# Performance work log

Hardware: AMD Instinct MI355X
Metric: run time of the kernel (lower is better)

## Reference

```python
import jax, jax.numpy as jnp
import numpy as np
import math

B, C, H, W, P = 8, 64, 256, 256, 16


def _conv2d(x, w, groups=1):
    # x: [B,C,H,W], w: [O, I/groups, kh, kw], 'SAME' padding, stride 1
    return jax.lax.conv_general_dilated(
        x, w, window_strides=(1, 1), padding='SAME',
        dimension_numbers=('NCHW', 'OIHW', 'NCHW'),
        feature_group_count=groups)


def _bn(x, g, b, m, v, eps=1e-5):
    # inference-mode BatchNorm2d over channel dim
    inv = jax.lax.rsqrt(v + eps)
    return (x - m[None, :, None, None]) * (g * inv)[None, :, None, None] + b[None, :, None, None]


def _layernorm(x, g, b, eps=1e-5):
    mu = x.mean(-1, keepdims=True)
    var = ((x - mu) ** 2).mean(-1, keepdims=True)
    return (x - mu) * jax.lax.rsqrt(var + eps) * g + b


def setup_inputs() -> dict:
    key = jax.random.key(0)
    ks = jax.random.split(key, 16)
    feat_map = jax.random.normal(ks[0], (B, C, H, W), jnp.float32)
    query = jax.random.normal(ks[1], (B, P, C), jnp.float32)
    key_tokens = jax.random.normal(ks[2], (B, H * W, C), jnp.float32)
    s = 1.0 / math.sqrt(C)
    dw_w = jax.random.normal(ks[3], (C, 1, 3, 3), jnp.float32) * (1.0 / 3.0)
    pw_w = jax.random.normal(ks[4], (C, C, 1, 1), jnp.float32) * s
    bn1_g = jnp.ones((C,)); bn1_b = jnp.zeros((C,))
    bn1_m = jnp.zeros((C,)); bn1_v = jnp.ones((C,))
    bn2_g = jnp.ones((C,)); bn2_b = jnp.zeros((C,))
    bn2_m = jnp.zeros((C,)); bn2_v = jnp.ones((C,))
    aff_w = jax.random.normal(ks[5], (P, C), jnp.float32) * s
    loc_w1 = jax.random.normal(ks[6], (C, C), jnp.float32) * s
    loc_b1 = jnp.zeros((C,))
    loc_w2 = jax.random.normal(ks[7], (C, C), jnp.float32) * s
    loc_b2 = jnp.zeros((C,))
    glb_w1 = jax.random.normal(ks[8], (C, C), jnp.float32) * s
    glb_b1 = jnp.zeros((C,))
    glb_w2 = jax.random.normal(ks[9], (C, C), jnp.float32) * s
    glb_b2 = jnp.zeros((C,))
    ln_g = jnp.ones((C,)); ln_b = jnp.zeros((C,))
    topo_scale = jnp.float32(0.01)
    orient_scale = jnp.float32(0.01)
    angles = jnp.linspace(0.0, math.pi, P + 1)[:-1]
    proto_orient = jnp.stack([jnp.cos(2.0 * angles), jnp.sin(2.0 * angles)], axis=1).astype(jnp.float32)
    return dict(feat_map=feat_map, query=query, key_tokens=key_tokens,
                dw_w=dw_w, bn1_g=bn1_g, bn1_b=bn1_b, bn1_m=bn1_m, bn1_v=bn1_v,
                pw_w=pw_w, bn2_g=bn2_g, bn2_b=bn2_b, bn2_m=bn2_m, bn2_v=bn2_v,
                aff_w=aff_w,
                loc_w1=loc_w1, loc_b1=loc_b1, loc_w2=loc_w2, loc_b2=loc_b2,
                glb_w1=glb_w1, glb_b1=glb_b1, glb_w2=glb_w2, glb_b2=glb_b2,
                ln_g=ln_g, ln_b=ln_b, topo_scale=topo_scale, orient_scale=orient_scale,
                proto_orient=proto_orient)


def reference(feat_map, query, key_tokens,
              dw_w, bn1_g, bn1_b, bn1_m, bn1_v,
              pw_w, bn2_g, bn2_b, bn2_m, bn2_v,
              aff_w,
              loc_w1, loc_b1, loc_w2, loc_b2,
              glb_w1, glb_b1, glb_w2, glb_b2,
              ln_g, ln_b, topo_scale, orient_scale, proto_orient):
    b, c, h, w = feat_map.shape
    hw = h * w
    # conv_spatial: depthwise 3x3 -> BN -> ReLU -> 1x1 -> BN -> ReLU
    x = _conv2d(feat_map, dw_w, groups=c)
    x = jax.nn.relu(_bn(x, bn1_g, bn1_b, bn1_m, bn1_v))
    x = _conv2d(x, pw_w)
    x = jax.nn.relu(_bn(x, bn2_g, bn2_b, bn2_m, bn2_v))
    feat_conv = x.reshape(b, c, hw).transpose(0, 2, 1)  # [B, L, C]
    # Sobel edge magnitude on channel-mean map
    edge_input = feat_map.mean(axis=1, keepdims=True)  # [B,1,H,W]
    sob_x = jnp.array([[-1, 0, 1], [-2, 0, 2], [-1, 0, 1]], jnp.float32).reshape(1, 1, 3, 3)
    sob_y = jnp.array([[-1, -2, -1], [0, 0, 0], [1, 2, 1]], jnp.float32).reshape(1, 1, 3, 3)
    gx = _conv2d(edge_input, sob_x)
    gy = _conv2d(edge_input, sob_y)
    edge_strength = jnp.sqrt(gx * gx + gy * gy + 1e-6)  # [B,1,H,W]
    # standardized edge weight over tokens (unbiased std, matching torch.std)
    ew = edge_strength.reshape(b, hw, 1)
    ew_mean = ew.mean(axis=1, keepdims=True)
    ew_var = ((ew - ew_mean) ** 2).sum(axis=1, keepdims=True) / (hw - 1)
    edge_weight = (ew - ew_mean) / (jnp.sqrt(ew_var) + 1e-5)  # [B,L,1]
    # doubled-angle orientation encoding
    gx2 = gx * gx
    gy2 = gy * gy
    denom = gx2 + gy2 + 1e-6
    ori_x = (gx2 - gy2) / denom
    ori_y = 2.0 * gx * gy / denom
    orient_tokens = jnp.concatenate([ori_x, ori_y], axis=1).reshape(b, 2, hw).transpose(0, 2, 1)  # [B,L,2]
    edge_conf = edge_strength.reshape(b, hw, 1)
    edge_conf = edge_conf / (edge_conf.mean(axis=1, keepdims=True) + 1e-6)
    edge_conf = jnp.clip(edge_conf, 0.0, 3.0)
    # prototype orientation bias
    proto_dirs = proto_orient / jnp.maximum(
        jnp.linalg.norm(proto_orient, axis=-1, keepdims=True), 1e-12)
    orient_scores = jnp.einsum('blc,pc->blp', orient_tokens, proto_dirs)
    orient_bias = orient_scores * edge_conf  # [B,L,P]
    raw_affinity = jnp.einsum('blc,pc->blp', feat_conv, aff_w)
    affinity_logits = raw_affinity + topo_scale * edge_weight + orient_scale * orient_bias
    affinity = jax.nn.softmax(affinity_logits, axis=1)  # softmax over tokens L
    prototypes = jnp.einsum('blp,blc->bpc', affinity, key_tokens)  # [B,P,C]
    # Contextual Significance Weighting gate
    z = prototypes + query
    loc = jax.nn.relu(z @ loc_w1.T + loc_b1) @ loc_w2.T + loc_b2
    g_ctx = z.mean(axis=1, keepdims=True)
    glb = jax.nn.relu(g_ctx @ glb_w1.T + glb_b1) @ glb_w2.T + glb_b2
    attn_weights = jax.nn.sigmoid(loc + glb)
    out = _layernorm(query * attn_weights + query, ln_g, ln_b)
    return out
```

## Files before the change

kernel.cpp:

```cpp
#include <hip/hip_runtime.h>
#include <hip/hip_fp16.h>
#include <math.h>

#define HW     65536
#define WIDTH  256
#define HEIGHT 256

typedef __attribute__((ext_vector_type(8))) short bf16x8;
typedef __attribute__((ext_vector_type(4))) float f32x4;

__device__ __forceinline__ float relu_f(float x){ return x > 0.f ? x : 0.f; }
__device__ __forceinline__ unsigned int f2bf(float x){
    union { float f; unsigned int u; } v; v.f = x;
    unsigned int r = v.u + 0x7fffu + ((v.u >> 16) & 1u);
    return r >> 16;
}
__device__ __forceinline__ float bfbits2f(unsigned int lo16){
    union { unsigned int u; float f; } v; v.u = lo16 << 16; return v.f;
}
__device__ __forceinline__ float h2f(unsigned int bits16){
    __half h = *(__half*)&bits16; return __half2float(h);
}

__global__ void k_prep(const float* __restrict__ pw_w, const float* __restrict__ aff_w,
                       const float* __restrict__ g1, const float* __restrict__ b1,
                       const float* __restrict__ m1, const float* __restrict__ v1,
                       const float* __restrict__ g2, const float* __restrict__ b2,
                       const float* __restrict__ m2, const float* __restrict__ v2,
                       float* __restrict__ scsh, unsigned short* __restrict__ pwA,
                       unsigned short* __restrict__ affA){
    int t = threadIdx.x;
    for (int i = t; i < 4096; i += 256){
        int e = i & 7, l = (i >> 3) & 63, ks = (i >> 9) & 1, ct = i >> 10;
        int co = ct * 16 + (l & 15);
        int ci = ks * 32 + (l >> 4) * 8 + e;
        pwA[i] = (unsigned short)f2bf(pw_w[co * 64 + ci]);
    }
    for (int i = t; i < 1024; i += 256){
        int e = i & 7, l = (i >> 3) & 63, ks = i >> 9;
        int p = l & 15, k = ks * 32 + (l >> 4) * 8 + e;
        affA[i] = (unsigned short)f2bf(aff_w[p * 64 + k]);
    }
    if (t < 64){
        float s = g1[t] * rsqrtf(v1[t] + 1e-5f);
        scsh[t]       = s;
        scsh[64 + t]  = b1[t] - m1[t] * s;
        float s2 = g2[t] * rsqrtf(v2[t] + 1e-5f);
        scsh[128 + t] = s2;
        scsh[192 + t] = b2[t] - m2[t] * s2;
    }
}

__global__ __launch_bounds__(256, 4) void k_conv_aff(
    const float* __restrict__ feat, const float* __restrict__ dw_w,
    const float* __restrict__ scsh, const unsigned short* __restrict__ pwA,
    const unsigned short* __restrict__ affA,
    unsigned short* __restrict__ logitsH, float* __restrict__ ei)
{
    __shared__ unsigned short x1u[256 * 68];
    __shared__ float eibuf[4][256];
    int t = threadIdx.x;
    int lane = t & 63;
    int wu = __builtin_amdgcn_readfirstlane(t >> 6);
    int orig = blockIdx.x;
    int flat = (orig & 7) * 256 + (orig >> 3);
    int b = flat >> 8, h = flat & 255;

    const bf16x8* pwA8 = (const bf16x8*)pwA;
    bf16x8 apw0 = pwA8[(wu * 2 + 0) * 64 + lane];
    bf16x8 apw1 = pwA8[(wu * 2 + 1) * 64 + lane];
    const bf16x8* affA8 = (const bf16x8*)affA;
    bf16x8 aaf0 = affA8[lane];
    bf16x8 aaf1 = affA8[64 + lane];
    int lcol = lane & 15, pq = lane >> 4;
    int cb = wu * 16 + pq * 4;
    float4 sc2v = *(const float4*)(scsh + 128 + cb);
    float4 sh2v = *(const float4*)(scsh + 192 + cb);

    int px0 = lane * 4;
    const float* fb = feat + (size_t)b * 64 * HW;
    int hh0 = (h > 0) ? h - 1 : 0;
    int hh2 = (h < 255) ? h + 1 : 255;
    float rw0 = (h > 0) ? 1.f : 0.f;
    float rw2 = (h < 255) ? 1.f : 0.f;
    int   roff0 = hh0 * WIDTH, roff1 = h * WIDTH, roff2 = hh2 * WIDTH;
    float mx = 0.f, my = 0.f, mz = 0.f, mw = 0.f;
    int swz = ((lane >> 2) & 7) << 1;
    #pragma unroll
    for (int cp = 0; cp < 8; cp++){
        int ci0 = wu * 16 + cp * 2;
        int ci1 = ci0 + 1;
        const float* base0 = fb + (size_t)ci0 * HW + px0;
        const float* base1 = fb + (size_t)ci1 * HW + px0;
        float a00=0.f,a01=0.f,a02=0.f,a03=0.f, a10=0.f,a11=0.f,a12=0.f,a13=0.f;
        #pragma unroll
        for (int r = 0; r < 3; r++){
            int roff = (r == 0) ? roff0 : ((r == 1) ? roff1 : roff2);
            float rwf = (r == 0) ? rw0 : ((r == 1) ? 1.f : rw2);
            float4 v0 = *(const float4*)(base0 + roff);
            float4 v1 = *(const float4*)(base1 + roff);
            float w00 = dw_w[ci0*9 + r*3 + 0] * rwf;
            float w01 = dw_w[ci0*9 + r*3 + 1] * rwf;
            float w02 = dw_w[ci0*9 + r*3 + 2] * rwf;
            float w10 = dw_w[ci1*9 + r*3 + 0] * rwf;
            float w11 = dw_w[ci1*9 + r*3 + 1] * rwf;
            float w12 = dw_w[ci1*9 + r*3 + 2] * rwf;
            float lf0 = __shfl_up(v0.w, 1);  if (lane == 0)  lf0 = 0.f;
            float rt0 = __shfl_down(v0.x, 1); if (lane == 63) rt0 = 0.f;
            float lf1 = __shfl_up(v1.w, 1);  if (lane == 0)  lf1 = 0.f;
            float rt1 = __shfl_down(v1.x, 1); if (lane == 63) rt1 = 0.f;
            a00 += lf0*w00 + v0.x*w01 + v0.y*w02;
            a01 += v0.x*w00 + v0.y*w01 + v0.z*w02;
            a02 += v0.y*w00 + v0.z*w01 + v0.w*w02;
            a03 += v0.z*w00 + v0.w*w01 + rt0*w02;
            a10 += lf1*w10 + v1.x*w11 + v1.y*w12;
            a11 += v1.x*w10 + v1.y*w11 + v1.z*w12;
            a12 += v1.y*w10 + v1.z*w11 + v1.w*w12;
            a13 += v1.z*w10 + v1.w*w11 + rt1*w12;
            if (r == 1){
                mx += v0.x + v1.x; my += v0.y + v1.y;
                mz += v0.z + v1.z; mw += v0.w + v1.w;
            }
        }
        float s0 = scsh[ci0], o0 = scsh[64 + ci0];
        float s1 = scsh[ci1], o1 = scsh[64 + ci1];
        int dwi = ((wu * 8 + cp) ^ swz) * 2;
        unsigned int pk0 = f2bf(relu_f(fmaf(a00,s0,o0))) | (f2bf(relu_f(fmaf(a10,s1,o1))) << 16);
        unsigned int pk1 = f2bf(relu_f(fmaf(a01,s0,o0))) | (f2bf(relu_f(fmaf(a11,s1,o1))) << 16);
        unsigned int pk2 = f2bf(relu_f(fmaf(a02,s0,o0))) | (f2bf(relu_f(fmaf(a12,s1,o1))) << 16);
        unsigned int pk3 = f2bf(relu_f(fmaf(a03,s0,o0))) | (f2bf(relu_f(fmaf(a13,s1,o1))) << 16);
        *(unsigned int*)&x1u[(px0 + 0) * 68 + dwi] = pk0;
        *(unsigned int*)&x1u[(px0 + 1) * 68 + dwi] = pk1;
        *(unsigned int*)&x1u[(px0 + 2) * 68 + dwi] = pk2;
        *(unsigned int*)&x1u[(px0 + 3) * 68 + dwi] = pk3;
    }
    *(float4*)&eibuf[wu][px0] = make_float4(mx, my, mz, mw);
    __syncthreads();
    {
        float m = (eibuf[0][t] + eibuf[1][t]) + (eibuf[2][t] + eibuf[3][t]);
        ei[(size_t)b * HW + h * WIDTH + t] = m * (1.f / 64.f);
    }

    int k0d = pq * 4;
    #pragma unroll
    for (int half = 0; half < 2; half++){
        f32x4 accB[8];
        #pragma unroll
        for (int q = 0; q < 8; q++){
            int jt = half * 8 + q;
            int swzj = (jt & 7) << 1;
            const unsigned short* rowp = &x1u[(jt * 16 + lcol) * 68];
            union { bf16x8 v; uint2 u[2]; } b0, b1;
            b0.u[0] = *(const uint2*)&rowp[((k0d)          ^ swzj) * 2];
            b0.u[1] = *(const uint2*)&rowp[((k0d + 2)      ^ swzj) * 2];
            b1.u[0] = *(const uint2*)&rowp[((16 + k0d)     ^ swzj) * 2];
            b1.u[1] = *(const uint2*)&rowp[((16 + k0d + 2) ^ swzj) * 2];
            f32x4 acc = {0.f, 0.f, 0.f, 0.f};
            acc = __builtin_amdgcn_mfma_f32_16x16x32_bf16(apw0, b0.v, acc, 0, 0, 0);
            acc = __builtin_amdgcn_mfma_f32_16x16x32_bf16(apw1, b1.v, acc, 0, 0, 0);
            accB[q] = acc;
        }
        __syncthreads();
        #pragma unroll
        for (int q = 0; q < 8; q++){
            int jt = half * 8 + q;
            int swzj = (jt & 7) << 1;
            f32x4 acc = accB[q];
            unsigned int y0 = f2bf(relu_f(fmaf(acc[0], sc2v.x, sh2v.x)))
                            | (f2bf(relu_f(fmaf(acc[1], sc2v.y, sh2v.y))) << 16);
            unsigned int y1 = f2bf(relu_f(fmaf(acc[2], sc2v.z, sh2v.z)))
                            | (f2bf(relu_f(fmaf(acc[3], sc2v.w, sh2v.w))) << 16);
            int D = (wu * 8 + pq * 2) ^ swzj;
            *(uint2*)&x1u[(jt * 16 + lcol) * 68 + D * 2] = make_uint2(y0, y1);
        }
    }
    __syncthreads();

    int p0 = pq * 4;
    #pragma unroll
    for (int q = 0; q < 4; q++){
        int jt = wu * 4 + q;
        int swzj = (jt & 7) << 1;
        const unsigned short* rowp = &x1u[(jt * 16 + lcol) * 68];
        union { bf16x8 v; uint2 u[2]; } b0, b1;
        b0.u[0] = *(const uint2*)&rowp[((k0d)          ^ swzj) * 2];
        b0.u[1] = *(const uint2*)&rowp[((k0d + 2)      ^ swzj) * 2];
        b1.u[0] = *(const uint2*)&rowp[((16 + k0d)     ^ swzj) * 2];
        b1.u[1] = *(const uint2*)&rowp[((16 + k0d + 2) ^ swzj) * 2];
        f32x4 acc = {0.f, 0.f, 0.f, 0.f};
        acc = __builtin_amdgcn_mfma_f32_16x16x32_bf16(aaf0, b0.v, acc, 0, 0, 0);
        acc = __builtin_amdgcn_mfma_f32_16x16x32_bf16(aaf1, b1.v, acc, 0, 0, 0);
        int gx = h * WIDTH + jt * 16 + lcol;
        __half h0 = __float2half(acc[0]), h1v = __float2half(acc[1]);
        __half h2 = __float2half(acc[2]), h3v = __float2half(acc[3]);
        unsigned int u0 = (unsigned int)(*(unsigned short*)&h0)
                        | ((unsigned int)(*(unsigned short*)&h1v) << 16);
        unsigned int u1 = (unsigned int)(*(unsigned short*)&h2)
                        | ((unsigned int)(*(unsigned short*)&h3v) << 16);
        *(uint2*)&logitsH[((size_t)b * HW + gx) * 16 + p0] = make_uint2(u0, u1);
    }
}

__global__ __launch_bounds__(256) void k_sobel_stats(const float* __restrict__ ei,
                                                     float* __restrict__ part){
    int ch = blockIdx.x, b = blockIdx.y, t = threadIdx.x;
    int lane = t & 63, w = t >> 6;
    int h = ch * 4 + w;
    int px0 = lane * 4;
    const float* e = ei + (size_t)b * HW;
    int hh0 = (h > 0) ? h - 1 : 0;
    int hh2 = (h < 255) ? h + 1 : 255;
    float rw0 = (h > 0) ? 1.f : 0.f;
    float rw2 = (h < 255) ? 1.f : 0.f;
    float4 v0 = *(const float4*)(e + hh0 * WIDTH + px0);
    float4 v1 = *(const float4*)(e + h   * WIDTH + px0);
    float4 v2 = *(const float4*)(e + hh2 * WIDTH + px0);
    v0.x *= rw0; v0.y *= rw0; v0.z *= rw0; v0.w *= rw0;
    v2.x *= rw2; v2.y *= rw2; v2.z *= rw2; v2.w *= rw2;
    float l0 = __shfl_up(v0.w, 1);   if (lane == 0)  l0 = 0.f;
    float r0 = __shfl_down(v0.x, 1); if (lane == 63) r0 = 0.f;
    float l1 = __shfl_up(v1.w, 1);   if (lane == 0)  l1 = 0.f;
    float r1 = __shfl_down(v1.x, 1); if (lane == 63) r1 = 0.f;
    float l2 = __shfl_up(v2.w, 1);   if (lane == 0)  l2 = 0.f;
    float r2 = __shfl_down(v2.x, 1); if (lane == 63) r2 = 0.f;
    float t0[6]  = {l0, v0.x, v0.y, v0.z, v0.w, r0};
    float m1a[6] = {l1, v1.x, v1.y, v1.z, v1.w, r1};
    float b2a[6] = {l2, v2.x, v2.y, v2.z, v2.w, r2};
    float s1 = 0.f, s2 = 0.f;
    #pragma unroll
    for (int j = 0; j < 4; j++){
        float gx = (t0[j+2] - t0[j]) + 2.f*(m1a[j+2] - m1a[j]) + (b2a[j+2] - b2a[j]);
        float gy = (b2a[j] + 2.f*b2a[j+1] + b2a[j+2]) - (t0[j] + 2.f*t0[j+1] + t0[j+2]);
        float esv = sqrtf(gx*gx + gy*gy + 1e-6f);
        s1 += esv; s2 += esv * esv;
    }
    #pragma unroll
    for (int off = 32; off >= 1; off >>= 1){
        s1 += __shfl_xor(s1, off, 64);
        s2 += __shfl_xor(s2, off, 64);
    }
    __shared__ float rs1[4], rs2[4];
    if (lane == 0){ rs1[w] = s1; rs2[w] = s2; }
    __syncthreads();
    if (t == 0)
        part[(b*64+ch)*2]     = (rs1[0] + rs1[1]) + (rs1[2] + rs1[3]);
    if (t == 1)
        part[(b*64+ch)*2 + 1] = (rs2[0] + rs2[1]) + (rs2[2] + rs2[3]);
}

__global__ __launch_bounds__(256) void k_smproto(
    const unsigned short* __restrict__ logitsH, const float* __restrict__ ei,
    const float* __restrict__ part, const float* __restrict__ proto_orient,
    const float* __restrict__ topo_s, const float* __restrict__ orient_s,
    const float* __restrict__ key,
    float* __restrict__ smpart, float* __restrict__ ppart)
{
    int ch = blockIdx.x, b = blockIdx.y, t = threadIdx.x;
    __shared__ float eit[4][258];
    __shared__ float sstat[3];
    __shared__ float pdl[32];
    __shared__ float Ml[16];
    __shared__ float rm[4][16], rs[4][16];
    __shared__ unsigned int wlds[512][10];

    for (int i = t; i < 1024; i += 256){
        int r = i >> 8, c = i & 255;
        int row = 2 * ch - 1 + r;
        eit[r][c + 1] = (row >= 0 && row < 256) ? ei[(size_t)b * HW + row * 256 + c] : 0.f;
    }
    if (t >= 128 && t < 136){
        int q = t - 128;
        eit[q >> 1][(q & 1) * 257] = 0.f;
    }
    if (t < 64){
        float s1 = part[(b*64 + t)*2], s2 = part[(b*64 + t)*2 + 1];
        #pragma unroll
        for (int off = 32; off >= 1; off >>= 1){
            s1 += __shfl_xor(s1, off, 64);
            s2 += __shfl_xor(s2, off, 64);
        }
        if (t == 0){
            float mean = s1 / 65536.f;
            float var = (s2 - 65536.f * mean * mean) / 65535.f;
            var = var > 0.f ? var : 0.f;
            sstat[0] = mean;
            sstat[1] = 1.f / (sqrtf(var) + 1e-5f);
            sstat[2] = 1.f / (mean + 1e-6f);
        }
    } else if (t >= 64 && t < 80){
        int p = t - 64;
        float nx = proto_orient[p*2], ny = proto_orient[p*2+1];
        float n = sqrtf(nx*nx + ny*ny);
        n = n > 1e-12f ? n : 1e-12f;
        pdl[p*2] = nx / n; pdl[p*2+1] = ny / n;
    }
    __syncthreads();
    float mean = sstat[0], rstd = sstat[1], cinv = sstat[2];
    float topo = topo_s[0], orient = orient_s[0];

    float m[16], s[16];
    #pragma unroll
    for (int p = 0; p < 16; p++){ m[p] = -1e30f; s[p] = 0.f; }
    uint4 pkA0, pkA1, pkB0, pkB1;
    {
        size_t gl0 = ((size_t)b * HW + ch * 512 + t) * 16;
        size_t gl1 = ((size_t)b * HW + ch * 512 + 256 + t) * 16;
        pkA0 = *(const uint4*)&logitsH[gl0];
        pkA1 = *(const uint4*)&logitsH[gl0 + 8];
        pkB0 = *(const uint4*)&logitsH[gl1];
        pkB1 = *(const uint4*)&logitsH[gl1 + 8];
    }
    float ewv[2], oxv[2], oyv[2];
    #pragma unroll
    for (int i = 0; i < 2; i++){
        int hl = i + 1, w = t;
        float vmm = eit[hl-1][w], vm0 = eit[hl-1][w+1], vmp = eit[hl-1][w+2];
        float v0m = eit[hl][w],                          v0p = eit[hl][w+2];
        float vpm = eit[hl+1][w], vp0 = eit[hl+1][w+1], vpp = eit[hl+1][w+2];
        float gx = vmp - vmm + 2.f*(v0p - v0m) + vpp - vpm;
        float gy = vpm + 2.f*vp0 + vpp - vmm - 2.f*vm0 - vmp;
        float denom = gx*gx + gy*gy + 1e-6f;
        float esv = sqrtf(denom);
        float cf = fminf(fmaxf(esv * cinv, 0.f), 3.f);
        ewv[i] = (esv - mean) * rstd;
        oxv[i] = ((gx*gx - gy*gy) / denom) * cf;
        oyv[i] = (2.f * gx * gy / denom) * cf;
        const uint4& q0 = (i == 0) ? pkA0 : pkB0;
        const uint4& q1 = (i == 0) ? pkA1 : pkB1;
        unsigned int wv[8] = {q0.x, q0.y, q0.z, q0.w, q1.x, q1.y, q1.z, q1.w};
        #pragma unroll
        for (int p = 0; p < 16; p++){
            unsigned int bits = (p & 1) ? (wv[p >> 1] >> 16) : (wv[p >> 1] & 0xffffu);
            float x = h2f(bits) + topo * ewv[i]
                    + orient * (oxv[i]*pdl[p*2] + oyv[i]*pdl[p*2+1]);
            float mn = fmaxf(m[p], x);
            s[p] = s[p] * __expf(m[p] - mn) + __expf(x - mn);
            m[p] = mn;
        }
    }
    #pragma unroll
    for (int p = 0; p < 16; p++){
        #pragma unroll
        for (int off = 32; off >= 1; off >>= 1){
            float m2 = __shfl_xor(m[p], off, 64);
            float s2v = __shfl_xor(s[p], off, 64);
            float mn = fmaxf(m[p], m2);
            s[p] = s[p] * __expf(m[p] - mn) + s2v * __expf(m2 - mn);
            m[p] = mn;
        }
    }
    int wid = t >> 6;
    if ((t & 63) == 0){
        #pragma unroll
        for (int p = 0; p < 16; p++){ rm[wid][p] = m[p]; rs[wid][p] = s[p]; }
    }
    __syncthreads();
    if (t < 16){
        float M = -1e30f, S = 0.f;
        #pragma unroll
        for (int w2 = 0; w2 < 4; w2++){
            float mw = rm[w2][t], sw2 = rs[w2][t];
            float mn = fmaxf(M, mw);
            S = S * __expf(M - mn) + sw2 * __expf(mw - mn);
            M = mn;
        }
        smpart[((b*16 + t)*128 + ch)*2]     = M;
        smpart[((b*16 + t)*128 + ch)*2 + 1] = S;
        Ml[t] = M;
    }
    __syncthreads();
    float Mloc[16];
    #pragma unroll
    for (int p = 0; p < 16; p++) Mloc[p] = Ml[p];

    #pragma unroll
    for (int i = 0; i < 2; i++){
        int tok = i * 256 + t;
        const uint4& q0 = (i == 0) ? pkA0 : pkB0;
        const uint4& q1 = (i == 0) ? pkA1 : pkB1;
        unsigned int wv[8] = {q0.x, q0.y, q0.z, q0.w, q1.x, q1.y, q1.z, q1.w};
        #pragma unroll
        for (int p2 = 0; p2 < 8; p2++){
            int pa = p2*2, pb2 = p2*2 + 1;
            float xa = h2f(wv[p2] & 0xffffu) + topo*ewv[i]
                     + orient*(oxv[i]*pdl[pa*2]  + oyv[i]*pdl[pa*2+1]);
            float xb = h2f(wv[p2] >> 16) + topo*ewv[i]
                     + orient*(oxv[i]*pdl[pb2*2] + oyv[i]*pdl[pb2*2+1]);
            wlds[tok][p2] = f2bf(__expf(xa - Mloc[pa])) | (f2bf(__expf(xb - Mloc[pb2])) << 16);
        }
    }
    __syncthreads();

    int w = t >> 6, lane = t & 63, cg = lane & 15, g = lane >> 4;
    const float4* kp = (const float4*)key + ((size_t)b * HW + ch * 512 + w * 128) * 16;
    float acc[16][4];
    #pragma unroll
    for (int p = 0; p < 16; p++)
        #pragma unroll
        for (int i = 0; i < 4; i++) acc[p][i] = 0.f;
    #pragma unroll 4
    for (int blk = 0; blk < 32; blk++){
        int tok = blk * 4 + g;
        float4 kv = kp[tok * 16 + cg];
        const unsigned int* wp = &wlds[w * 128 + tok][0];
        uint2 q0 = *(const uint2*)&wp[0];
        uint2 q1 = *(const uint2*)&wp[2];
        uint2 q2 = *(const uint2*)&wp[4];
        uint2 q3 = *(const uint2*)&wp[6];
        unsigned int ww[8] = {q0.x, q0.y, q1.x, q1.y, q2.x, q2.y, q3.x, q3.y};
        #pragma unroll
        for (int p2 = 0; p2 < 8; p2++){
            float wa = bfbits2f(ww[p2] & 0xffffu);
            float wb = bfbits2f(ww[p2] >> 16);
            int pa = 2*p2, pb2 = 2*p2 + 1;
            acc[pa][0] = fmaf(wa, kv.x, acc[pa][0]);
            acc[pa][1] = fmaf(wa, kv.y, acc[pa][1]);
            acc[pa][2] = fmaf(wa, kv.z, acc[pa][2]);
            acc[pa][3] = fmaf(wa, kv.w, acc[pa][3]);
            acc[pb2][0] = fmaf(wb, kv.x, acc[pb2][0]);
            acc[pb2][1] = fmaf(wb, kv.y, acc[pb2][1]);
            acc[pb2][2] = fmaf(wb, kv.z, acc[pb2][2]);
            acc[pb2][3] = fmaf(wb, kv.w, acc[pb2][3]);
        }
    }
    #pragma unroll
    for (int p = 0; p < 16; p++)
        #pragma unroll
        for (int i = 0; i < 4; i++){
            acc[p][i] += __shfl_xor(acc[p][i], 16, 64);
            acc[p][i] += __shfl_xor(acc[p][i], 32, 64);
        }
    __syncthreads();
    float (*red)[16][68] = (float (*)[16][68])wlds;
    if (g == 0){
        #pragma unroll
        for (int p = 0; p < 16; p++)
            *(float4*)&red[w][p][cg*4] =
                make_float4(acc[p][0], acc[p][1], acc[p][2], acc[p][3]);
    }
    __syncthreads();
    size_t obase = ((size_t)(b * 128 + ch)) * 1024;
    for (int idx = t; idx < 1024; idx += 256){
        int p = idx >> 6, c = idx & 63;
        ppart[obase + idx] = red[0][p][c] + red[1][p][c] + red[2][p][c] + red[3][p][c];
    }
}

__global__ __launch_bounds__(256) void k_reduce(
    const float* __restrict__ smpart, const float* __restrict__ ppart,
    float* __restrict__ proto)
{
    int p = blockIdx.x, b = blockIdx.y, t = threadIdx.x;
    __shared__ float arr[128], flv[128], partial[4][64];
    float Mt = -1e30f, St = 0.f;
    if (t < 128){
        Mt = smpart[((b*16 + p)*128 + t)*2];
        St = smpart[((b*16 + p)*128 + t)*2 + 1];
        arr[t] = Mt;
    }
    __syncthreads();
    for (int s = 64; s > 0; s >>= 1){
        if (t < s) arr[t] = fmaxf(arr[t], arr[t + s]);
        __syncthreads();
    }
    float M = arr[0];
    __syncthreads();
    if (t < 128) arr[t] = St * __expf(Mt - M);
    __syncthreads();
    for (int s = 64; s > 0; s >>= 1){
        if (t < s) arr[t] += arr[t + s];
        __syncthreads();
    }
    float Stot = arr[0];
    __syncthreads();
    if (t < 128) flv[t] = __expf(Mt - M) / Stot;
    __syncthreads();
    int c = t & 63, half = t >> 6;
    float acc = 0.f;
    #pragma unroll 8
    for (int j = 0; j < 32; j++){
        int ch = half * 32 + j;
        acc += flv[ch] * ppart[((size_t)(b * 128 + ch)) * 1024 + p * 64 + c];
    }
    partial[half][c] = acc;
    __syncthreads();
    if (t < 64)
        proto[b * 1024 + p * 64 + t] =
            (partial[0][t] + partial[1][t]) + (partial[2][t] + partial[3][t]);
}

__global__ __launch_bounds__(256) void k_gate(
    const float* __restrict__ proto, const float* __restrict__ query,
    const float* __restrict__ w1, const float* __restrict__ bb1,
    const float* __restrict__ w2, const float* __restrict__ bb2,
    const float* __restrict__ gw1, const float* __restrict__ gb1,
    const float* __restrict__ gw2, const float* __restrict__ gb2,
    const float* __restrict__ lng, const float* __restrict__ lnb,
    float* __restrict__ out)
{
    __shared__ float z[16][64], h1[16][64], loc[16][64], g[64], hg[64], glb[64];
    int b = blockIdx.x, t = threadIdx.x;
    for (int idx = t; idx < 1024; idx += 256)
        z[idx >> 6][idx & 63] = proto[b * 1024 + idx] + query[b * 1024 + idx];
    __syncthreads();
    for (int idx = t; idx < 1024; idx += 256){
        int p = idx >> 6, j = idx & 63;
        float acc = bb1[j];
        for (int i = 0; i < 64; i++) acc += z[p][i] * w1[j * 64 + i];
        h1[p][j] = relu_f(acc);
    }
    if (t < 64){
        float sg = 0.f;
        for (int p = 0; p < 16; p++) sg += z[p][t];
        g[t] = sg * (1.f / 16.f);
    }
    __syncthreads();
    for (int idx = t; idx < 1024; idx += 256){
        int p = idx >> 6, k = idx & 63;
        float acc = bb2[k];
        for (int j = 0; j < 64; j++) acc += h1[p][j] * w2[k * 64 + j];
        loc[p][k] = acc;
    }
    if (t < 64){
        float acc = gb1[t];
        for (int i = 0; i < 64; i++) acc += g[i] * gw1[t * 64 + i];
        hg[t] = relu_f(acc);
    }
    __syncthreads();
    if (t < 64){
        float acc = gb2[t];
        for (int j = 0; j < 64; j++) acc += hg[j] * gw2[t * 64 + j];
        glb[t] = acc;
    }
    __syncthreads();
    for (int idx = t; idx < 1024; idx += 256){
        int p = idx >> 6, c = idx & 63;
        float a = loc[p][c] + glb[c];
        float sg = 1.f / (1.f + expf(-a));
        float q = query[b * 1024 + idx];
        h1[p][c] = q * sg + q;
    }
    __syncthreads();
    if (t < 16){
        int p = t;
        float mu = 0.f;
        for (int c = 0; c < 64; c++) mu += h1[p][c];
        mu *= (1.f / 64.f);
        float var = 0.f;
        for (int c = 0; c < 64; c++){ float d = h1[p][c] - mu; var += d * d; }
        var *= (1.f / 64.f);
        float rstd = rsqrtf(var + 1e-5f);
        for (int c = 0; c < 64; c++)
            out[b * 1024 + p * 64 + c] = (h1[p][c] - mu) * rstd * lng[c] + lnb[c];
    }
}

extern "C" void kernel_launch(void* const* d_in, const int* in_sizes, int n_in,
                              void* d_out, int out_size, void* d_ws, size_t ws_size,
                              hipStream_t stream){
    (void)in_sizes; (void)n_in; (void)out_size; (void)ws_size;
    const float* feat   = (const float*)d_in[0];
    const float* query  = (const float*)d_in[1];
    const float* key    = (const float*)d_in[2];
    const float* dw_w   = (const float*)d_in[3];
    const float* bn1_g  = (const float*)d_in[4];
    const float* bn1_b  = (const float*)d_in[5];
    const float* bn1_m  = (const float*)d_in[6];
    const float* bn1_v  = (const float*)d_in[7];
    const float* pw_w   = (const float*)d_in[8];
    const float* bn2_g  = (const float*)d_in[9];
    const float* bn2_b  = (const float*)d_in[10];
    const float* bn2_m  = (const float*)d_in[11];
    const float* bn2_v  = (const float*)d_in[12];
    const float* aff_w  = (const float*)d_in[13];
    const float* loc_w1 = (const float*)d_in[14];
    const float* loc_b1 = (const float*)d_in[15];
    const float* loc_w2 = (const float*)d_in[16];
    const float* loc_b2 = (const float*)d_in[17];
    const float* glb_w1 = (const float*)d_in[18];
    const float* glb_b1 = (const float*)d_in[19];
    const float* glb_w2 = (const float*)d_in[20];
    const float* glb_b2 = (const float*)d_in[21];
    const float* ln_g   = (const float*)d_in[22];
    const float* ln_b   = (const float*)d_in[23];
    const float* topo   = (const float*)d_in[24];
    const float* orient = (const float*)d_in[25];
    const float* proto_orient = (const float*)d_in[26];
    float* out = (float*)d_out;
    float* ws  = (float*)d_ws;

    float* ei      = ws;
    unsigned short* logitsH = (unsigned short*)(ws + 1048576);
    float* ppart   = ws + 5242880;
    float* k3part  = ws + 6291456;
    float* smpart  = ws + 6292480;
    float* proto   = ws + 6325248;
    float* scsh    = ws + 6333440;
    unsigned short* pwA  = (unsigned short*)(ws + 6333696);
    unsigned short* affA = (unsigned short*)(ws + 6335744);

    k_prep<<<1, 256, 0, stream>>>(pw_w, aff_w, bn1_g, bn1_b, bn1_m, bn1_v,
                                  bn2_g, bn2_b, bn2_m, bn2_v, scsh, pwA, affA);
    k_conv_aff<<<2048, 256, 0, stream>>>(feat, dw_w, scsh, pwA, affA, logitsH, ei);
    k_sobel_stats<<<dim3(64, 8), 256, 0, stream>>>(ei, k3part);
    k_smproto<<<dim3(128, 8), 256, 0, stream>>>(logitsH, ei, k3part, proto_orient,
                                                topo, orient, key, smpart, ppart);
    k_reduce<<<dim3(16, 8), 256, 0, stream>>>(smpart, ppart, proto);
    k_gate<<<8, 256, 0, stream>>>(proto, query, loc_w1, loc_b1, loc_w2, loc_b2,
                                  glb_w1, glb_b1, glb_w2, glb_b2, ln_g, ln_b, out);
}
```

Measured before the change: 128.2 us.

## Prefetch conv rows, two-pass softmax in smproto, fold reduce into gate kernel

The depthwise conv loop now loads the next channel pair's three rows while the current pair is computed, a register double buffer meant to hide global load latency. k_smproto replaces its online max/sum softmax with a two-pass scheme: a block max first, then exponentials computed once and reused for both the sum and the LDS weights. It also gets a launch-bounds occupancy hint. The separate k_reduce kernel is removed and its cross-chunk softmax merge and prototype reduction move into k_gate, saving a launch but running that reduction over only 8 blocks.

```diff
diff --git a/kernel.cpp b/kernel.cpp
--- a/kernel.cpp
+++ b/kernel.cpp
@@ -86,19 +86,38 @@
     int   roff0 = hh0 * WIDTH, roff1 = h * WIDTH, roff2 = hh2 * WIDTH;
     float mx = 0.f, my = 0.f, mz = 0.f, mw = 0.f;
     int swz = ((lane >> 2) & 7) << 1;
+
+    float4 cur0[3], cur1[3], nxt0[3], nxt1[3];
+    {
+        const float* p0 = fb + (size_t)(wu * 16) * HW + px0;
+        const float* p1 = p0 + HW;
+        cur0[0] = *(const float4*)(p0 + roff0);
+        cur0[1] = *(const float4*)(p0 + roff1);
+        cur0[2] = *(const float4*)(p0 + roff2);
+        cur1[0] = *(const float4*)(p1 + roff0);
+        cur1[1] = *(const float4*)(p1 + roff1);
+        cur1[2] = *(const float4*)(p1 + roff2);
+    }
     #pragma unroll
     for (int cp = 0; cp < 8; cp++){
         int ci0 = wu * 16 + cp * 2;
         int ci1 = ci0 + 1;
-        const float* base0 = fb + (size_t)ci0 * HW + px0;
-        const float* base1 = fb + (size_t)ci1 * HW + px0;
+        if (cp < 7){
+            const float* p0 = fb + (size_t)(ci0 + 2) * HW + px0;
+            const float* p1 = p0 + HW;
+            nxt0[0] = *(const float4*)(p0 + roff0);
+            nxt0[1] = *(const float4*)(p0 + roff1);
+            nxt0[2] = *(const float4*)(p0 + roff2);
+            nxt1[0] = *(const float4*)(p1 + roff0);
+            nxt1[1] = *(const float4*)(p1 + roff1);
+            nxt1[2] = *(const float4*)(p1 + roff2);
+        }
         float a00=0.f,a01=0.f,a02=0.f,a03=0.f, a10=0.f,a11=0.f,a12=0.f,a13=0.f;
         #pragma unroll
         for (int r = 0; r < 3; r++){
-            int roff = (r == 0) ? roff0 : ((r == 1) ? roff1 : roff2);
             float rwf = (r == 0) ? rw0 : ((r == 1) ? 1.f : rw2);
-            float4 v0 = *(const float4*)(base0 + roff);
-            float4 v1 = *(const float4*)(base1 + roff);
+            float4 v0 = cur0[r];
+            float4 v1 = cur1[r];
             float w00 = dw_w[ci0*9 + r*3 + 0] * rwf;
             float w01 = dw_w[ci0*9 + r*3 + 1] * rwf;
             float w02 = dw_w[ci0*9 + r*3 + 2] * rwf;
@@ -133,6 +152,8 @@
         *(unsigned int*)&x1u[(px0 + 1) * 68 + dwi] = pk1;
         *(unsigned int*)&x1u[(px0 + 2) * 68 + dwi] = pk2;
         *(unsigned int*)&x1u[(px0 + 3) * 68 + dwi] = pk3;
+        #pragma unroll
+        for (int r = 0; r < 3; r++){ cur0[r] = nxt0[r]; cur1[r] = nxt1[r]; }
     }
     *(float4*)&eibuf[wu][px0] = make_float4(mx, my, mz, mw);
     __syncthreads();
@@ -248,7 +269,7 @@
         part[(b*64+ch)*2 + 1] = (rs2[0] + rs2[1]) + (rs2[2] + rs2[3]);
 }
 
-__global__ __launch_bounds__(256) void k_smproto(
+__global__ __launch_bounds__(256, 4) void k_smproto(
     const unsigned short* __restrict__ logitsH, const float* __restrict__ ei,
     const float* __restrict__ part, const float* __restrict__ proto_orient,
     const float* __restrict__ topo_s, const float* __restrict__ orient_s,
@@ -298,9 +319,7 @@
     float mean = sstat[0], rstd = sstat[1], cinv = sstat[2];
     float topo = topo_s[0], orient = orient_s[0];
 
-    float m[16], s[16];
-    #pragma unroll
-    for (int p = 0; p < 16; p++){ m[p] = -1e30f; s[p] = 0.f; }
+    float xv0[16], xv1[16];
     uint4 pkA0, pkA1, pkB0, pkB1;
     {
         size_t gl0 = ((size_t)b * HW + ch * 512 + t) * 16;
@@ -310,7 +329,6 @@
         pkB0 = *(const uint4*)&logitsH[gl1];
         pkB1 = *(const uint4*)&logitsH[gl1 + 8];
     }
-    float ewv[2], oxv[2], oyv[2];
     #pragma unroll
     for (int i = 0; i < 2; i++){
         int hl = i + 1, w = t;
@@ -322,74 +340,68 @@
         float denom = gx*gx + gy*gy + 1e-6f;
         float esv = sqrtf(denom);
         float cf = fminf(fmaxf(esv * cinv, 0.f), 3.f);
-        ewv[i] = (esv - mean) * rstd;
-        oxv[i] = ((gx*gx - gy*gy) / denom) * cf;
-        oyv[i] = (2.f * gx * gy / denom) * cf;
+        float ew = (esv - mean) * rstd;
+        float oxv = ((gx*gx - gy*gy) / denom) * cf;
+        float oyv = (2.f * gx * gy / denom) * cf;
         const uint4& q0 = (i == 0) ? pkA0 : pkB0;
         const uint4& q1 = (i == 0) ? pkA1 : pkB1;
         unsigned int wv[8] = {q0.x, q0.y, q0.z, q0.w, q1.x, q1.y, q1.z, q1.w};
+        float* xv = (i == 0) ? xv0 : xv1;
         #pragma unroll
         for (int p = 0; p < 16; p++){
             unsigned int bits = (p & 1) ? (wv[p >> 1] >> 16) : (wv[p >> 1] & 0xffffu);
-            float x = h2f(bits) + topo * ewv[i]
-                    + orient * (oxv[i]*pdl[p*2] + oyv[i]*pdl[p*2+1]);
-            float mn = fmaxf(m[p], x);
-            s[p] = s[p] * __expf(m[p] - mn) + __expf(x - mn);
-            m[p] = mn;
-        }
-    }
+            xv[p] = h2f(bits) + topo * ew + orient * (oxv*pdl[p*2] + oyv*pdl[p*2+1]);
+        }
+    }
+    float mxr[16];
     #pragma unroll
     for (int p = 0; p < 16; p++){
-        #pragma unroll
-        for (int off = 32; off >= 1; off >>= 1){
-            float m2 = __shfl_xor(m[p], off, 64);
-            float s2v = __shfl_xor(s[p], off, 64);
-            float mn = fmaxf(m[p], m2);
-            s[p] = s[p] * __expf(m[p] - mn) + s2v * __expf(m2 - mn);
-            m[p] = mn;
-        }
+        float m = fmaxf(xv0[p], xv1[p]);
+        #pragma unroll
+        for (int off = 32; off >= 1; off >>= 1)
+            m = fmaxf(m, __shfl_xor(m, off, 64));
+        mxr[p] = m;
     }
     int wid = t >> 6;
     if ((t & 63) == 0){
         #pragma unroll
-        for (int p = 0; p < 16; p++){ rm[wid][p] = m[p]; rs[wid][p] = s[p]; }
+        for (int p = 0; p < 16; p++) rm[wid][p] = mxr[p];
+    }
+    __syncthreads();
+    if (t < 16)
+        Ml[t] = fmaxf(fmaxf(rm[0][t], rm[1][t]), fmaxf(rm[2][t], rm[3][t]));
+    __syncthreads();
+    float Mloc[16];
+    #pragma unroll
+    for (int p = 0; p < 16; p++) Mloc[p] = Ml[p];
+
+    float e0[16], e1[16], sthr[16];
+    #pragma unroll
+    for (int p = 0; p < 16; p++){
+        e0[p] = __expf(xv0[p] - Mloc[p]);
+        e1[p] = __expf(xv1[p] - Mloc[p]);
+        sthr[p] = e0[p] + e1[p];
+    }
+    #pragma unroll
+    for (int p2 = 0; p2 < 8; p2++){
+        wlds[t][p2]       = f2bf(e0[2*p2]) | (f2bf(e0[2*p2+1]) << 16);
+        wlds[256 + t][p2] = f2bf(e1[2*p2]) | (f2bf(e1[2*p2+1]) << 16);
+    }
+    #pragma unroll
+    for (int p = 0; p < 16; p++){
+        #pragma unroll
+        for (int off = 32; off >= 1; off >>= 1)
+            sthr[p] += __shfl_xor(sthr[p], off, 64);
+    }
+    if ((t & 63) == 0){
+        #pragma unroll
+        for (int p = 0; p < 16; p++) rs[wid][p] = sthr[p];
     }
     __syncthreads();
     if (t < 16){
-        float M = -1e30f, S = 0.f;
-        #pragma unroll
-        for (int w2 = 0; w2 < 4; w2++){
-            float mw = rm[w2][t], sw2 = rs[w2][t];
-            float mn = fmaxf(M, mw);
-            S = S * __expf(M - mn) + sw2 * __expf(mw - mn);
-            M = mn;
-        }
-        smpart[((b*16 + t)*128 + ch)*2]     = M;
-        smpart[((b*16 + t)*128 + ch)*2 + 1] = S;
-        Ml[t] = M;
-    }
-    __syncthreads();
-    float Mloc[16];
-    #pragma unroll
-    for (int p = 0; p < 16; p++) Mloc[p] = Ml[p];
-
-    #pragma unroll
-    for (int i = 0; i < 2; i++){
-        int tok = i * 256 + t;
-        const uint4& q0 = (i == 0) ? pkA0 : pkB0;
-        const uint4& q1 = (i == 0) ? pkA1 : pkB1;
-        unsigned int wv[8] = {q0.x, q0.y, q0.z, q0.w, q1.x, q1.y, q1.z, q1.w};
-        #pragma unroll
-        for (int p2 = 0; p2 < 8; p2++){
-            int pa = p2*2, pb2 = p2*2 + 1;
-            float xa = h2f(wv[p2] & 0xffffu) + topo*ewv[i]
-                     + orient*(oxv[i]*pdl[pa*2]  + oyv[i]*pdl[pa*2+1]);
-            float xb = h2f(wv[p2] >> 16) + topo*ewv[i]
-                     + orient*(oxv[i]*pdl[pb2*2] + oyv[i]*pdl[pb2*2+1]);
-            wlds[tok][p2] = f2bf(__expf(xa - Mloc[pa])) | (f2bf(__expf(xb - Mloc[pb2])) << 16);
-        }
-    }
-    __syncthreads();
+        smpart[((b*16 + t)*128 + ch)*2]     = Ml[t];
+        smpart[((b*16 + t)*128 + ch)*2 + 1] = (rs[0][t] + rs[1][t]) + (rs[2][t] + rs[3][t]);
+    }
 
     int w = t >> 6, lane = t & 63, cg = lane & 15, g = lane >> 4;
     const float4* kp = (const float4*)key + ((size_t)b * HW + ch * 512 + w * 128) * 16;
@@ -446,51 +458,9 @@
     }
 }
 
-__global__ __launch_bounds__(256) void k_reduce(
+__global__ __launch_bounds__(256) void k_gate(
     const float* __restrict__ smpart, const float* __restrict__ ppart,
-    float* __restrict__ proto)
-{
-    int p = blockIdx.x, b = blockIdx.y, t = threadIdx.x;
-    __shared__ float arr[128], flv[128], partial[4][64];
-    float Mt = -1e30f, St = 0.f;
-    if (t < 128){
-        Mt = smpart[((b*16 + p)*128 + t)*2];
-        St = smpart[((b*16 + p)*128 + t)*2 + 1];
-        arr[t] = Mt;
-    }
-    __syncthreads();
-    for (int s = 64; s > 0; s >>= 1){
-        if (t < s) arr[t] = fmaxf(arr[t], arr[t + s]);
-        __syncthreads();
-    }
-    float M = arr[0];
-    __syncthreads();
-    if (t < 128) arr[t] = St * __expf(Mt - M);
-    __syncthreads();
-    for (int s = 64; s > 0; s >>= 1){
-        if (t < s) arr[t] += arr[t + s];
-        __syncthreads();
-    }
-    float Stot = arr[0];
-    __syncthreads();
-    if (t < 128) flv[t] = __expf(Mt - M) / Stot;
-    __syncthreads();
-    int c = t & 63, half = t >> 6;
-    float acc = 0.f;
-    #pragma unroll 8
-    for (int j = 0; j < 32; j++){
-        int ch = half * 32 + j;
-        acc += flv[ch] * ppart[((size_t)(b * 128 + ch)) * 1024 + p * 64 + c];
-    }
-    partial[half][c] = acc;
-    __syncthreads();
-    if (t < 64)
-        proto[b * 1024 + p * 64 + t] =
-            (partial[0][t] + partial[1][t]) + (partial[2][t] + partial[3][t]);
-}
-
-__global__ __launch_bounds__(256) void k_gate(
-    const float* __restrict__ proto, const float* __restrict__ query,
+    const float* __restrict__ query,
     const float* __restrict__ w1, const float* __restrict__ bb1,
     const float* __restrict__ w2, const float* __restrict__ bb2,
     const float* __restrict__ gw1, const float* __restrict__ gb1,
@@ -499,9 +469,44 @@
     float* __restrict__ out)
 {
     __shared__ float z[16][64], h1[16][64], loc[16][64], g[64], hg[64], glb[64];
+    __shared__ float flv[16][128];
     int b = blockIdx.x, t = threadIdx.x;
-    for (int idx = t; idx < 1024; idx += 256)
-        z[idx >> 6][idx & 63] = proto[b * 1024 + idx] + query[b * 1024 + idx];
+    {
+        int p = t >> 4, j = t & 15;
+        const float* sp = smpart + ((size_t)(b*16 + p)) * 256;
+        float M = -1e30f, S = 0.f;
+        #pragma unroll
+        for (int k = 0; k < 8; k++){
+            int ch = j*8 + k;
+            float mw = sp[ch*2], sw = sp[ch*2 + 1];
+            float mn = fmaxf(M, mw);
+            S = S * __expf(M - mn) + sw * __expf(mw - mn);
+            M = mn;
+        }
+        #pragma unroll
+        for (int off = 8; off >= 1; off >>= 1){
+            float m2 = __shfl_xor(M, off, 64);
+            float s2 = __shfl_xor(S, off, 64);
+            float mn = fmaxf(M, m2);
+            S = S * __expf(M - mn) + s2 * __expf(m2 - mn);
+            M = mn;
+        }
+        float rinv = 1.f / S;
+        #pragma unroll
+        for (int k = 0; k < 8; k++){
+            int ch = j*8 + k;
+            flv[p][ch] = __expf(sp[ch*2] - M) * rinv;
+        }
+    }
+    __syncthreads();
+    for (int idx = t; idx < 1024; idx += 256){
+        int p = idx >> 6;
+        const float* pp = ppart + (size_t)b * 128 * 1024 + idx;
+        float sacc = 0.f;
+        #pragma unroll 8
+        for (int ch = 0; ch < 128; ch++) sacc += flv[p][ch] * pp[(size_t)ch * 1024];
+        z[p][idx & 63] = sacc + query[b * 1024 + idx];
+    }
     __syncthreads();
     for (int idx = t; idx < 1024; idx += 256){
         int p = idx >> 6, j = idx & 63;
@@ -594,7 +599,6 @@
     float* ppart   = ws + 5242880;
     float* k3part  = ws + 6291456;
     float* smpart  = ws + 6292480;
-    float* proto   = ws + 6325248;
     float* scsh    = ws + 6333440;
     unsigned short* pwA  = (unsigned short*)(ws + 6333696);
     unsigned short* affA = (unsigned short*)(ws + 6335744);
@@ -605,7 +609,6 @@
     k_sobel_stats<<<dim3(64, 8), 256, 0, stream>>>(ei, k3part);
     k_smproto<<<dim3(128, 8), 256, 0, stream>>>(logitsH, ei, k3part, proto_orient,
                                                 topo, orient, key, smpart, ppart);
-    k_reduce<<<dim3(16, 8), 256, 0, stream>>>(smpart, ppart, proto);
-    k_gate<<<8, 256, 0, stream>>>(proto, query, loc_w1, loc_b1, loc_w2, loc_b2,
+    k_gate<<<8, 256, 0, stream>>>(smpart, ppart, query, loc_w1, loc_b1, loc_w2, loc_b2,
                                   glb_w1, glb_b1, glb_w2, glb_b2, ln_g, ln_b, out);
 }
```

After: 233.2 us. +81.9%, slower.
